# Performance work log

Measured on AMD Instinct MI355X. Metric: run time of the kernel, lower is better.

Reference implementation:

```python
import jax, jax.numpy as jnp
import numpy as np

HEADS = 24
HEAD_DIM = 128
DIM = HEADS * HEAD_DIM  # 3072
EPS = 1e-5


def _rms_norm(x, w):
    # x: [B,S,H,D], w: [D]
    var = jnp.mean(jnp.square(x), axis=-1, keepdims=True)
    return x * jax.lax.rsqrt(var + EPS) * w


def _apply_rope(x, cos, sin):
    # non-neox (interleaved pairs): x: [B,S,H,D], cos/sin: [S,D]
    B, S, H, D = x.shape
    xr = x.reshape(B, S, H, D // 2, 2)
    x_real, x_imag = xr[..., 0], xr[..., 1]
    rotated = jnp.stack([-x_imag, x_real], axis=-1).reshape(B, S, H, D)
    c = cos[None, :, None, :]
    s = sin[None, :, None, :]
    return x * c + rotated * s


def setup_inputs() -> dict:
    key = jax.random.key(0)
    ks = jax.random.split(key, 20)
    B, S_img, S_txt = 1, 2048, 512
    S = S_img + S_txt
    sc = 1.0 / np.sqrt(DIM)
    inp = {
        "x": jax.random.normal(ks[0], (B, S_img, DIM), jnp.float32),
        "encoder_hidden_states": jax.random.normal(ks[1], (B, S_txt, DIM), jnp.float32),
        "rope_cos": jax.random.uniform(ks[2], (S, HEAD_DIM), jnp.float32),
        "rope_sin": jax.random.uniform(ks[3], (S, HEAD_DIM), jnp.float32),
        # image-stream projections (bias=False)
        "wq": jax.random.normal(ks[4], (DIM, DIM), jnp.float32) * sc,
        "wk": jax.random.normal(ks[5], (DIM, DIM), jnp.float32) * sc,
        "wv": jax.random.normal(ks[6], (DIM, DIM), jnp.float32) * sc,
        # text-stream projections (added_proj_bias=True)
        "w_add_q": jax.random.normal(ks[7], (DIM, DIM), jnp.float32) * sc,
        "w_add_k": jax.random.normal(ks[8], (DIM, DIM), jnp.float32) * sc,
        "w_add_v": jax.random.normal(ks[9], (DIM, DIM), jnp.float32) * sc,
        "b_add_q": jax.random.normal(ks[10], (DIM,), jnp.float32) * 0.01,
        "b_add_k": jax.random.normal(ks[11], (DIM,), jnp.float32) * 0.01,
        "b_add_v": jax.random.normal(ks[12], (DIM,), jnp.float32) * 0.01,
        # per-head RMSNorm weights
        "norm_q_w": jnp.ones((HEAD_DIM,), jnp.float32),
        "norm_k_w": jnp.ones((HEAD_DIM,), jnp.float32),
        "norm_aq_w": jnp.ones((HEAD_DIM,), jnp.float32),
        "norm_ak_w": jnp.ones((HEAD_DIM,), jnp.float32),
        # output projections (out_bias=True)
        "w_out": jax.random.normal(ks[13], (DIM, DIM), jnp.float32) * sc,
        "b_out": jax.random.normal(ks[14], (DIM,), jnp.float32) * 0.01,
        "w_add_out": jax.random.normal(ks[15], (DIM, DIM), jnp.float32) * sc,
        "b_add_out": jax.random.normal(ks[16], (DIM,), jnp.float32) * 0.01,
    }
    return inp


def reference(x, encoder_hidden_states, rope_cos, rope_sin,
              wq, wk, wv, w_add_q, w_add_k, w_add_v,
              b_add_q, b_add_k, b_add_v,
              norm_q_w, norm_k_w, norm_aq_w, norm_ak_w,
              w_out, b_out, w_add_out, b_add_out):
    B, S_img, _ = x.shape
    S_txt = encoder_hidden_states.shape[1]

    def proj(h, w, b=None):
        y = jnp.einsum('bsd,ed->bse', h, w)
        return y if b is None else y + b

    def heads(t):
        return t.reshape(B, t.shape[1], HEADS, HEAD_DIM)

    q = _rms_norm(heads(proj(x, wq)), norm_q_w)
    k = _rms_norm(heads(proj(x, wk)), norm_k_w)
    v = heads(proj(x, wv))

    eq = _rms_norm(heads(proj(encoder_hidden_states, w_add_q, b_add_q)), norm_aq_w)
    ek = _rms_norm(heads(proj(encoder_hidden_states, w_add_k, b_add_k)), norm_ak_w)
    ev = heads(proj(encoder_hidden_states, w_add_v, b_add_v))

    # encoder tokens first, then image tokens
    q = jnp.concatenate([eq, q], axis=1)
    k = jnp.concatenate([ek, k], axis=1)
    v = jnp.concatenate([ev, v], axis=1)

    q = _apply_rope(q, rope_cos, rope_sin)
    k = _apply_rope(k, rope_cos, rope_sin)

    scale = 1.0 / np.sqrt(HEAD_DIM)
    scores = jnp.einsum('bqhd,bkhd->bhqk', q, k) * scale
    attn = jax.nn.softmax(scores, axis=-1)
    o = jnp.einsum('bhqk,bkhd->bqhd', attn, v)
    o = o.reshape(B, S_txt + S_img, DIM)

    enc_o, img_o = o[:, :S_txt], o[:, S_txt:]
    img_out = jnp.einsum('bsd,ed->bse', img_o, w_out) + b_out
    enc_out = jnp.einsum('bsd,ed->bse', enc_o, w_add_out) + b_add_out
    return img_out, enc_out
```

## Files before the change

### kernel.cpp

```cpp
#include <hip/hip_runtime.h>
#include <hip/hip_bf16.h>


typedef __hip_bfloat16 bf16;
typedef __attribute__((ext_vector_type(8))) short short8;
typedef __attribute__((ext_vector_type(4))) short s16x4;
typedef __attribute__((ext_vector_type(4))) float f32x4;

#define KDIM 3072
#define S_TXT 512
#define S_IMG 2048
#define S_ALL 2560
#define NHEADS 24
#define HDIM 128
#define WELEM (KDIM * KDIM)
#define AELEM (S_ALL * KDIM)
#define NSPLIT 3

__device__ __forceinline__ void async_ld16(const void* g, void* l) {
  __builtin_amdgcn_global_load_lds((__attribute__((address_space(1))) void*)g,
                                   (__attribute__((address_space(3))) void*)l,
                                   16, 0, 0);
}

__device__ __forceinline__ short bf16_bits(float x) {
  bf16 h = (bf16)x;
  return __builtin_bit_cast(short, h);
}
__device__ __forceinline__ float bits_f32(short s) {
  return (float)__builtin_bit_cast(bf16, s);
}

__global__ __launch_bounds__(256) void cast_weights_kernel(
    const float* __restrict__ w0, const float* __restrict__ w1,
    const float* __restrict__ w2, const float* __restrict__ w3,
    const float* __restrict__ w4, const float* __restrict__ w5,
    const float* __restrict__ w6, const float* __restrict__ w7,
    bf16* __restrict__ dst) {
  const float* srcs[8] = {w0, w1, w2, w3, w4, w5, w6, w7};
  const float* __restrict__ src = srcs[blockIdx.y];
  bf16* __restrict__ out = dst + (size_t)blockIdx.y * WELEM;
  const size_t i0 = ((size_t)blockIdx.x * 256 + threadIdx.x) * 8;
  const float4 f0 = *(const float4*)(src + i0);
  const float4 f1 = *(const float4*)(src + i0 + 4);
  short8 o;
  o[0] = bf16_bits(f0.x); o[1] = bf16_bits(f0.y);
  o[2] = bf16_bits(f0.z); o[3] = bf16_bits(f0.w);
  o[4] = bf16_bits(f1.x); o[5] = bf16_bits(f1.y);
  o[6] = bf16_bits(f1.z); o[7] = bf16_bits(f1.w);
  *(short8*)(out + i0) = o;
}

__global__ __launch_bounds__(256) void cast_acts_kernel(
    const float* __restrict__ x, const float* __restrict__ enc,
    bf16* __restrict__ xe) {
  const size_t i0 = ((size_t)blockIdx.x * 256 + threadIdx.x) * 8;
  const size_t TXT = (size_t)S_TXT * KDIM;
  const float* __restrict__ src = (i0 < TXT) ? (enc + i0) : (x + (i0 - TXT));
  const float4 f0 = *(const float4*)(src);
  const float4 f1 = *(const float4*)(src + 4);
  short8 o;
  o[0] = bf16_bits(f0.x); o[1] = bf16_bits(f0.y);
  o[2] = bf16_bits(f0.z); o[3] = bf16_bits(f0.w);
  o[4] = bf16_bits(f1.x); o[5] = bf16_bits(f1.y);
  o[6] = bf16_bits(f1.z); o[7] = bf16_bits(f1.w);
  *(short8*)(xe + i0) = o;
}

template <typename OutT, bool TRANS>
__device__ __forceinline__ void gemm_tile(const bf16* __restrict__ A,
                                          const bf16* __restrict__ B,
                                          OutT* __restrict__ C,
                                          const float* __restrict__ bias) {
  __shared__ alignas(16) short sA[128 * 32];
  __shared__ alignas(16) short sB[128 * 32];
  const int tid = threadIdx.x;
  const int lane = tid & 63;
  const int w = tid >> 6;
  const int a = lane & 15;
  const int g = lane >> 4;
  const int wm = (w >> 1) * 64;
  const int wn = (w & 1) * 64;

  f32x4 acc[4][4] = {};

  const int s0 = tid, s1 = tid + 256;
  const int r0 = s0 >> 2, b0 = (s0 & 3) ^ ((r0 >> 1) & 3);
  const int r1 = s1 >> 2, b1 = (s1 & 3) ^ ((r1 >> 1) & 3);
  const bf16* gA0 = A + (size_t)r0 * KDIM + b0 * 8;
  const bf16* gA1 = A + (size_t)r1 * KDIM + b1 * 8;
  const bf16* gB0 = B + (size_t)r0 * KDIM + b0 * 8;
  const bf16* gB1 = B + (size_t)r1 * KDIM + b1 * 8;
  short* lA0 = sA + (w * 64) * 8;
  short* lA1 = sA + (256 + w * 64) * 8;
  short* lB0 = sB + (w * 64) * 8;
  short* lB1 = sB + (256 + w * 64) * 8;

  for (int k0 = 0; k0 < KDIM; k0 += 32) {
    __syncthreads();
    async_ld16(gA0 + k0, lA0);
    async_ld16(gA1 + k0, lA1);
    async_ld16(gB0 + k0, lB0);
    async_ld16(gB1 + k0, lB1);
    __syncthreads();
    short8 af[4], bfg[4];
#pragma unroll
    for (int i = 0; i < 4; i++) {
      const int R = wm + i * 16 + a;
      af[i] = *(const short8*)(sA + R * 32 + ((g ^ ((R >> 1) & 3)) * 8));
    }
#pragma unroll
    for (int j = 0; j < 4; j++) {
      const int R = wn + j * 16 + a;
      bfg[j] = *(const short8*)(sB + R * 32 + ((g ^ ((R >> 1) & 3)) * 8));
    }
#pragma unroll
    for (int i = 0; i < 4; i++)
#pragma unroll
      for (int j = 0; j < 4; j++)
        acc[i][j] = __builtin_amdgcn_mfma_f32_16x16x32_bf16(af[i], bfg[j], acc[i][j], 0, 0, 0);
  }

  if constexpr (TRANS) {
#pragma unroll
    for (int i = 0; i < 4; i++)
#pragma unroll
      for (int j = 0; j < 4; j++) {
        const int col = wn + j * 16 + a;
        const float bv = bias ? bias[col] : 0.0f;
        s16x4 pk;
#pragma unroll
        for (int r = 0; r < 4; r++) pk[r] = bf16_bits(acc[i][j][r] + bv);
        *(s16x4*)((short*)C + (size_t)col * S_ALL + wm + i * 16 + g * 4) = pk;
      }
  } else {
#pragma unroll
    for (int i = 0; i < 4; i++)
#pragma unroll
      for (int j = 0; j < 4; j++) {
        const int col = wn + j * 16 + a;
        const float bv = bias ? bias[col] : 0.0f;
#pragma unroll
        for (int r = 0; r < 4; r++) {
          const int row = wm + i * 16 + g * 4 + r;
          C[(size_t)row * KDIM + col] = (OutT)(acc[i][j][r] + bv);
        }
      }
  }
}

__global__ __launch_bounds__(256) void qkv_kernel(
    const bf16* __restrict__ XE, const bf16* __restrict__ Wc,
    const float* __restrict__ bq, const float* __restrict__ bk, const float* __restrict__ bv,
    bf16* __restrict__ Q, bf16* __restrict__ K, bf16* __restrict__ VT) {
  const int bm = blockIdx.x;
  const int bn = blockIdx.y;
  const int which = bn / 24;
  const int nc = (bn % 24) * 128;
  const bool txt = bm < 4;
  const bf16* W = Wc + (size_t)(txt ? (3 + which) : which) * WELEM + (size_t)nc * KDIM;
  const float* bias = nullptr;
  if (txt) bias = ((which == 0) ? bq : (which == 1) ? bk : bv) + nc;
  const int crow = bm * 128;
  const bf16* A = XE + (size_t)crow * KDIM;
  if (which == 2) {
    gemm_tile<bf16, true>(A, W, VT + (size_t)nc * S_ALL + crow, bias);
  } else {
    bf16* Out = (which == 0) ? Q : K;
    gemm_tile<bf16, false>(A, W, Out + (size_t)crow * KDIM + nc, bias);
  }
}

__global__ __launch_bounds__(256) void outproj_kernel(
    const bf16* __restrict__ Obuf, const bf16* __restrict__ Wc,
    const float* __restrict__ b_out, const float* __restrict__ b_add,
    float* __restrict__ out) {
  const int bm = blockIdx.x;
  const int bn = blockIdx.y;
  const bool txt = bm < 4;
  const bf16* A = Obuf + (size_t)bm * 128 * KDIM;
  const bf16* W = Wc + (size_t)(txt ? 7 : 6) * WELEM;
  const float* bias = txt ? b_add : b_out;
  float* C = txt ? (out + (size_t)S_IMG * KDIM + (size_t)bm * 128 * KDIM)
                 : (out + (size_t)(bm - 4) * 128 * KDIM);
  gemm_tile<float, false>(A, W + (size_t)bn * 128 * KDIM, C + bn * 128, bias + bn * 128);
}

__global__ __launch_bounds__(256) void norm_rope_kernel(
    bf16* __restrict__ Q, bf16* __restrict__ K,
    const float* __restrict__ rc, const float* __restrict__ rs,
    const float* __restrict__ nqw, const float* __restrict__ nkw,
    const float* __restrict__ naqw, const float* __restrict__ nakw) {
  const int row = blockIdx.x;
  const int h = blockIdx.y * 4 + (threadIdx.x >> 6);
  const int t = threadIdx.x & 63;
  const long base = (long)row * KDIM + h * HDIM;
  const int d0 = 2 * t, d1 = d0 + 1;
  const bool txt = row < S_TXT;
  const float QSCL = 0.08838834764831845f * 1.4426950408889634f;
  float qa = (float)Q[base + d0], qb = (float)Q[base + d1];
  float ka = (float)K[base + d0], kb = (float)K[base + d1];
  float sq = qa * qa + qb * qb;
  float sk = ka * ka + kb * kb;
#pragma unroll
  for (int m = 1; m < 64; m <<= 1) {
    sq += __shfl_xor(sq, m);
    sk += __shfl_xor(sk, m);
  }
  const float rq = rsqrtf(sq * (1.0f / 128.0f) + 1e-5f) * QSCL;
  const float rk = rsqrtf(sk * (1.0f / 128.0f) + 1e-5f);
  const float* qw = txt ? naqw : nqw;
  const float* kw = txt ? nakw : nkw;
  const float c0 = rc[row * HDIM + d0], c1 = rc[row * HDIM + d1];
  const float s0 = rs[row * HDIM + d0], s1 = rs[row * HDIM + d1];
  const float qn0 = qa * rq * qw[d0], qn1 = qb * rq * qw[d1];
  const float kn0 = ka * rk * kw[d0], kn1 = kb * rk * kw[d1];
  Q[base + d0] = (bf16)(qn0 * c0 - qn1 * s0);
  Q[base + d1] = (bf16)(qn1 * c1 + qn0 * s1);
  K[base + d0] = (bf16)(kn0 * c0 - kn1 * s0);
  K[base + d1] = (bf16)(kn1 * c1 + kn0 * s1);
}

__global__ __launch_bounds__(256) void flash_kernel(
    const bf16* __restrict__ Q, const bf16* __restrict__ Kb,
    const bf16* __restrict__ VT,
    bf16* __restrict__ Op0, bf16* __restrict__ Op1, bf16* __restrict__ Op2,
    float* __restrict__ L) {
  __shared__ alignas(16) short sK[64 * 128];
  __shared__ alignas(16) short sVT[128 * 64];
  __shared__ alignas(16) short sP[4][32 * 72];
  const int tid = threadIdx.x;
  const int lane = tid & 63;
  const int w = tid >> 6;
  const int a = lane & 15;
  const int g = lane >> 4;
  const int qt = blockIdx.x;
  const int h = blockIdx.y;
  const int split = blockIdx.z;
  const int it0 = split * 13;
  const int it1 = (split == 2) ? 40 : (it0 + 13);
  const int qrow0 = qt * 128 + w * 32;
  short* const sPw = sP[w];

  short8 qf[2][4];
#pragma unroll
  for (int mi = 0; mi < 2; mi++)
#pragma unroll
    for (int kk = 0; kk < 4; kk++)
      qf[mi][kk] = *(const short8*)(Q + (size_t)(qrow0 + mi * 16 + a) * KDIM + h * HDIM + kk * 32 + g * 8);

  f32x4 oacc[2][8] = {};
  float lsum[2] = {0.0f, 0.0f};

  for (int it = it0; it < it1; ++it) {
    const int kv0 = it * 64;
    __syncthreads();
#pragma unroll
    for (int is = 0; is < 4; is++) {
      const int s = is * 256 + w * 64 + lane;
      const int kr = s >> 4, p = s & 15;
      const int lb = (p - (kr & 7)) & 15;
      async_ld16(Kb + (size_t)(kv0 + kr) * KDIM + h * HDIM + lb * 8,
                 sK + (is * 256 + w * 64) * 8);
    }
#pragma unroll
    for (int is = 0; is < 4; is++) {
      const int s = is * 256 + w * 64 + lane;
      const int dr = s >> 3, p = s & 7;
      const int lb = (p - (dr & 7)) & 7;
      async_ld16(VT + (size_t)(h * HDIM + dr) * S_ALL + kv0 + lb * 8,
                 sVT + (is * 256 + w * 64) * 8);
    }
    __syncthreads();

    f32x4 st[4][2] = {};
#pragma unroll
    for (int kk = 0; kk < 4; kk++) {
      short8 kf[4];
#pragma unroll
      for (int ni = 0; ni < 4; ni++) {
        const int kr = ni * 16 + a;
        const int p = ((kk * 4 + g) + (kr & 7)) & 15;
        kf[ni] = *(const short8*)(sK + kr * 128 + p * 8);
      }
#pragma unroll
      for (int ni = 0; ni < 4; ni++)
#pragma unroll
        for (int mi = 0; mi < 2; mi++)
          st[ni][mi] = __builtin_amdgcn_mfma_f32_16x16x32_bf16(kf[ni], qf[mi][kk], st[ni][mi], 0, 0, 0);
    }

#pragma unroll
    for (int mi = 0; mi < 2; mi++)
#pragma unroll
      for (int ni = 0; ni < 4; ni++) {
        s16x4 pk;
#pragma unroll
        for (int r = 0; r < 4; r++) {
          const float p = exp2f(st[ni][mi][r]);
          lsum[mi] += p;
          pk[r] = bf16_bits(p);
        }
        *(s16x4*)(sPw + (mi * 16 + a) * 72 + ni * 16 + g * 4) = pk;
      }

#pragma unroll
    for (int ks = 0; ks < 2; ks++) {
      short8 pf[2];
#pragma unroll
      for (int mi = 0; mi < 2; mi++)
        pf[mi] = *(const short8*)(sPw + (mi * 16 + a) * 72 + ks * 32 + g * 8);
#pragma unroll
      for (int nd = 0; nd < 8; nd++) {
        const int dr = nd * 16 + a;
        const int p = ((ks * 4 + g) + (dr & 7)) & 7;
        const short8 vf = *(const short8*)(sVT + dr * 64 + p * 8);
#pragma unroll
        for (int mi = 0; mi < 2; mi++)
          oacc[mi][nd] = __builtin_amdgcn_mfma_f32_16x16x32_bf16(pf[mi], vf, oacc[mi][nd], 0, 0, 0);
      }
    }
  }

#pragma unroll
  for (int mi = 0; mi < 2; mi++) {
    lsum[mi] += __shfl_xor(lsum[mi], 16);
    lsum[mi] += __shfl_xor(lsum[mi], 32);
  }
  bf16* __restrict__ Op = (split == 0) ? Op0 : (split == 1) ? Op1 : Op2;
#pragma unroll
  for (int mi = 0; mi < 2; mi++) {
#pragma unroll
    for (int r = 0; r < 4; r++) {
      const float inv = 1.0f / __shfl(lsum[mi], g * 4 + r);
      const size_t row = qrow0 + mi * 16 + g * 4 + r;
#pragma unroll
      for (int nd = 0; nd < 8; nd++)
        Op[row * KDIM + h * HDIM + nd * 16 + a] = (bf16)(oacc[mi][nd][r] * inv);
    }
    if (g == 0)
      L[((size_t)split * NHEADS + h) * S_ALL + qrow0 + mi * 16 + a] = lsum[mi];
  }
}

__global__ __launch_bounds__(256) void merge_kernel(
    bf16* __restrict__ O0, const bf16* __restrict__ O1, const bf16* __restrict__ O2,
    const float* __restrict__ L) {
  const size_t i0 = ((size_t)blockIdx.x * 256 + threadIdx.x) * 8;
  const int row = (int)(i0 / KDIM);
  const int h = (int)((i0 % KDIM) >> 7);
  const float l0 = L[((size_t)0 * NHEADS + h) * S_ALL + row];
  const float l1 = L[((size_t)1 * NHEADS + h) * S_ALL + row];
  const float l2 = L[((size_t)2 * NHEADS + h) * S_ALL + row];
  const float inv = 1.0f / (l0 + l1 + l2);
  const float w0 = l0 * inv, w1 = l1 * inv, w2 = l2 * inv;
  const short8 v0 = *(const short8*)(O0 + i0);
  const short8 v1 = *(const short8*)(O1 + i0);
  const short8 v2 = *(const short8*)(O2 + i0);
  short8 o;
#pragma unroll
  for (int u = 0; u < 8; u++)
    o[u] = bf16_bits(w0 * bits_f32(v0[u]) + w1 * bits_f32(v1[u]) + w2 * bits_f32(v2[u]));
  *(short8*)(O0 + i0) = o;
}

extern "C" void kernel_launch(void* const* d_in, const int* in_sizes, int n_in,
                              void* d_out, int out_size, void* d_ws, size_t ws_size,
                              hipStream_t stream) {
  const float* x    = (const float*)d_in[0];
  const float* enc  = (const float*)d_in[1];
  const float* rc   = (const float*)d_in[2];
  const float* rs   = (const float*)d_in[3];
  const float* wq   = (const float*)d_in[4];
  const float* wk   = (const float*)d_in[5];
  const float* wv   = (const float*)d_in[6];
  const float* waq  = (const float*)d_in[7];
  const float* wak  = (const float*)d_in[8];
  const float* wav  = (const float*)d_in[9];
  const float* bq   = (const float*)d_in[10];
  const float* bk   = (const float*)d_in[11];
  const float* bv   = (const float*)d_in[12];
  const float* nqw  = (const float*)d_in[13];
  const float* nkw  = (const float*)d_in[14];
  const float* naqw = (const float*)d_in[15];
  const float* nakw = (const float*)d_in[16];
  const float* w_out     = (const float*)d_in[17];
  const float* b_out     = (const float*)d_in[18];
  const float* w_add_out = (const float*)d_in[19];
  const float* b_add_out = (const float*)d_in[20];

  bf16* Wc   = (bf16*)d_ws;
  bf16* XE   = Wc + (size_t)8 * WELEM;
  bf16* Q    = XE + AELEM;
  bf16* K    = Q + AELEM;
  bf16* VT   = K + AELEM;
  bf16* Obuf = VT + AELEM;
  bf16* Op1  = Obuf + AELEM;
  bf16* Op2  = XE;
  float* L   = (float*)(Op1 + AELEM);

  cast_weights_kernel<<<dim3(WELEM / 2048, 8), 256, 0, stream>>>(
      wq, wk, wv, waq, wak, wav, w_out, w_add_out, Wc);
  cast_acts_kernel<<<dim3(AELEM / 2048), 256, 0, stream>>>(x, enc, XE);

  qkv_kernel<<<dim3(20, 72), 256, 0, stream>>>(XE, Wc, bq, bk, bv, Q, K, VT);
  norm_rope_kernel<<<dim3(S_ALL, 6), 256, 0, stream>>>(Q, K, rc, rs, nqw, nkw, naqw, nakw);
  flash_kernel<<<dim3(20, NHEADS, NSPLIT), 256, 0, stream>>>(Q, K, VT, Obuf, Op1, Op2, L);
  merge_kernel<<<dim3(AELEM / 2048), 256, 0, stream>>>(Obuf, Op1, Op2, L);
  outproj_kernel<<<dim3(20, NHEADS), 256, 0, stream>>>(Obuf, Wc, b_out, b_add_out,
                                                       (float*)d_out);
}
```

Before: 754.0 us.

## Rewrite QKV GEMM as 256x256 tiled, 8-wave pipelined kernel with XCD block remap

```diff
diff --git a/kernel.cpp b/kernel.cpp
--- a/kernel.cpp
+++ b/kernel.cpp
@@ -16,6 +16,7 @@
 #define WELEM (KDIM * KDIM)
 #define AELEM (S_ALL * KDIM)
 #define NSPLIT 3
+#define NT_K 48
 
 __device__ __forceinline__ void async_ld16(const void* g, void* l) {
   __builtin_amdgcn_global_load_lds((__attribute__((address_space(1))) void*)g,
@@ -29,6 +30,17 @@
 }
 __device__ __forceinline__ float bits_f32(short s) {
   return (float)__builtin_bit_cast(bf16, s);
+}
+
+__device__ __forceinline__ void phase_mid() {
+  __builtin_amdgcn_s_barrier();
+  asm volatile("s_waitcnt lgkmcnt(0)" ::: "memory");
+  __builtin_amdgcn_sched_barrier(0);
+  __builtin_amdgcn_s_setprio(1);
+}
+__device__ __forceinline__ void phase_end() {
+  __builtin_amdgcn_s_setprio(0);
+  __builtin_amdgcn_s_barrier();
 }
 
 __global__ __launch_bounds__(256) void cast_weights_kernel(
@@ -68,6 +80,175 @@
 }
 
 template <typename OutT, bool TRANS>
+__device__ __forceinline__ void gemm256(const bf16* __restrict__ Ab,
+                                        const bf16* __restrict__ Bb,
+                                        OutT* __restrict__ C,
+                                        const float* __restrict__ bias,
+                                        short* sAmem, short* sBmem) {
+  const int tid = threadIdx.x;
+  const int lane = tid & 63;
+  const int w = tid >> 6;
+  const int a = lane & 15;
+  const int g = (lane >> 4) & 3;
+  const int wm = w >> 2;
+  const int wn = w & 3;
+
+  short* const A00 = sAmem;
+  short* const A01 = sAmem + 8192;
+  short* const A10 = sAmem + 16384;
+  short* const A11 = sAmem + 24576;
+  short* const B00 = sBmem;
+  short* const B01 = sBmem + 8192;
+  short* const B10 = sBmem + 16384;
+  short* const B11 = sBmem + 24576;
+
+  auto stage = [&](const bf16* gb, int kbase, short* lblk) {
+#pragma unroll
+    for (int l = 0; l < 2; l++) {
+      const int t = l * 512 + tid;
+      const int row = t >> 2;
+      const int ls = (t & 3) ^ ((row >> 1) & 3);
+      async_ld16(gb + (size_t)row * KDIM + kbase + ls * 8,
+                 lblk + (l * 512 + w * 64) * 8);
+    }
+  };
+  auto frag = [&](const short* lblk, int R) -> short8 {
+    return *(const short8*)(lblk + R * 32 + ((g ^ ((R >> 1) & 3)) * 8));
+  };
+
+  f32x4 acc[8][4] = {};
+
+  stage(Bb, 0, B00);
+  stage(Ab, 0, A00);
+  stage(Bb, 32, B01);
+  stage(Ab, 32, A01);
+  stage(Bb, 64, B10);
+  stage(Ab, 64, A10);
+  stage(Bb, 96, B11);
+  asm volatile("s_waitcnt vmcnt(6)" ::: "memory");
+  __builtin_amdgcn_s_barrier();
+
+  const int ra = wm * 128 + a;
+  const int rb = wn * 64 + a;
+
+  auto kblock = [&](int u, short* cA0, short* cA1, short* cB0, short* cB1,
+                    short* nA1) {
+    short8 af[4], bfr[4];
+#pragma unroll
+    for (int i = 0; i < 4; i++) af[i] = frag(cA0, ra + i * 16);
+#pragma unroll
+    for (int j = 0; j < 4; j++) bfr[j] = frag(cB0, rb + j * 16);
+    if (u + 1 < NT_K) stage(Ab, (u + 1) * 64 + 32, nA1);
+    phase_mid();
+#pragma unroll
+    for (int i = 0; i < 4; i++)
+#pragma unroll
+      for (int j = 0; j < 4; j++)
+        acc[i][j] = __builtin_amdgcn_mfma_f32_16x16x32_bf16(af[i], bfr[j], acc[i][j], 0, 0, 0);
+    phase_end();
+#pragma unroll
+    for (int i = 0; i < 4; i++) af[i] = frag(cA0, ra + (i + 4) * 16);
+    if (u + 2 < NT_K) stage(Bb, (u + 2) * 64, cB0);
+    phase_mid();
+#pragma unroll
+    for (int i = 0; i < 4; i++)
+#pragma unroll
+      for (int j = 0; j < 4; j++)
+        acc[i + 4][j] = __builtin_amdgcn_mfma_f32_16x16x32_bf16(af[i], bfr[j], acc[i + 4][j], 0, 0, 0);
+    phase_end();
+#pragma unroll
+    for (int i = 0; i < 4; i++) af[i] = frag(cA1, ra + i * 16);
+#pragma unroll
+    for (int j = 0; j < 4; j++) bfr[j] = frag(cB1, rb + j * 16);
+    if (u + 2 < NT_K) stage(Ab, (u + 2) * 64, cA0);
+    phase_mid();
+#pragma unroll
+    for (int i = 0; i < 4; i++)
+#pragma unroll
+      for (int j = 0; j < 4; j++)
+        acc[i][j] = __builtin_amdgcn_mfma_f32_16x16x32_bf16(af[i], bfr[j], acc[i][j], 0, 0, 0);
+    phase_end();
+#pragma unroll
+    for (int i = 0; i < 4; i++) af[i] = frag(cA1, ra + (i + 4) * 16);
+    if (u + 2 < NT_K) stage(Bb, (u + 2) * 64 + 32, cB1);
+    __builtin_amdgcn_s_barrier();
+    asm volatile("s_waitcnt lgkmcnt(0)" ::: "memory");
+    __builtin_amdgcn_sched_barrier(0);
+    __builtin_amdgcn_s_setprio(1);
+#pragma unroll
+    for (int i = 0; i < 4; i++)
+#pragma unroll
+      for (int j = 0; j < 4; j++)
+        acc[i + 4][j] = __builtin_amdgcn_mfma_f32_16x16x32_bf16(af[i], bfr[j], acc[i + 4][j], 0, 0, 0);
+    __builtin_amdgcn_s_setprio(0);
+    if (u < NT_K - 2)
+      asm volatile("s_waitcnt vmcnt(6)" ::: "memory");
+    else
+      asm volatile("s_waitcnt vmcnt(0)" ::: "memory");
+    __builtin_amdgcn_s_barrier();
+  };
+
+#pragma unroll 1
+  for (int u = 0; u < NT_K; u += 2) {
+    kblock(u,     A00, A01, B00, B01, A11);
+    kblock(u + 1, A10, A11, B10, B11, A01);
+  }
+
+  if constexpr (TRANS) {
+#pragma unroll
+    for (int i = 0; i < 8; i++)
+#pragma unroll
+      for (int j = 0; j < 4; j++) {
+        const int col = wn * 64 + j * 16 + a;
+        const float bv = bias ? bias[col] : 0.0f;
+        s16x4 pk;
+#pragma unroll
+        for (int r = 0; r < 4; r++) pk[r] = bf16_bits(acc[i][j][r] + bv);
+        *(s16x4*)((short*)C + (size_t)col * S_ALL + wm * 128 + i * 16 + g * 4) = pk;
+      }
+  } else {
+#pragma unroll
+    for (int i = 0; i < 8; i++)
+#pragma unroll
+      for (int j = 0; j < 4; j++) {
+        const int col = wn * 64 + j * 16 + a;
+        const float bv = bias ? bias[col] : 0.0f;
+#pragma unroll
+        for (int r = 0; r < 4; r++) {
+          const int row = wm * 128 + i * 16 + g * 4 + r;
+          C[(size_t)row * KDIM + col] = (OutT)(acc[i][j][r] + bv);
+        }
+      }
+  }
+}
+
+__global__ __launch_bounds__(512, 2) void qkv_kernel(
+    const bf16* __restrict__ XE, const bf16* __restrict__ Wc,
+    const float* __restrict__ bq, const float* __restrict__ bk, const float* __restrict__ bv,
+    bf16* __restrict__ Q, bf16* __restrict__ K, bf16* __restrict__ VT) {
+  __shared__ alignas(16) short sAmem[4 * 8192];
+  __shared__ alignas(16) short sBmem[4 * 8192];
+  const int bid = blockIdx.x;
+  const int wk_ = (bid & 7) * 45 + (bid >> 3);
+  const int bm = wk_ / 36;
+  const int bn = wk_ % 36;
+  const int which = bn / 12;
+  const int nc = (bn % 12) * 256;
+  const bool txt = bm < 2;
+  const bf16* W = Wc + (size_t)(txt ? (3 + which) : which) * WELEM + (size_t)nc * KDIM;
+  const float* bias = nullptr;
+  if (txt) bias = ((which == 0) ? bq : (which == 1) ? bk : bv) + nc;
+  const int crow = bm * 256;
+  const bf16* A = XE + (size_t)crow * KDIM;
+  if (which == 2) {
+    gemm256<bf16, true>(A, W, VT + (size_t)nc * S_ALL + crow, bias, sAmem, sBmem);
+  } else {
+    bf16* Out = (which == 0) ? Q : K;
+    gemm256<bf16, false>(A, W, Out + (size_t)crow * KDIM + nc, bias, sAmem, sBmem);
+  }
+}
+
+template <typename OutT, bool TRANS>
 __device__ __forceinline__ void gemm_tile(const bf16* __restrict__ A,
                                           const bf16* __restrict__ B,
                                           OutT* __restrict__ C,
@@ -146,28 +327,6 @@
           C[(size_t)row * KDIM + col] = (OutT)(acc[i][j][r] + bv);
         }
       }
-  }
-}
-
-__global__ __launch_bounds__(256) void qkv_kernel(
-    const bf16* __restrict__ XE, const bf16* __restrict__ Wc,
-    const float* __restrict__ bq, const float* __restrict__ bk, const float* __restrict__ bv,
-    bf16* __restrict__ Q, bf16* __restrict__ K, bf16* __restrict__ VT) {
-  const int bm = blockIdx.x;
-  const int bn = blockIdx.y;
-  const int which = bn / 24;
-  const int nc = (bn % 24) * 128;
-  const bool txt = bm < 4;
-  const bf16* W = Wc + (size_t)(txt ? (3 + which) : which) * WELEM + (size_t)nc * KDIM;
-  const float* bias = nullptr;
-  if (txt) bias = ((which == 0) ? bq : (which == 1) ? bk : bv) + nc;
-  const int crow = bm * 128;
-  const bf16* A = XE + (size_t)crow * KDIM;
-  if (which == 2) {
-    gemm_tile<bf16, true>(A, W, VT + (size_t)nc * S_ALL + crow, bias);
-  } else {
-    bf16* Out = (which == 0) ? Q : K;
-    gemm_tile<bf16, false>(A, W, Out + (size_t)crow * KDIM + nc, bias);
   }
 }
 
@@ -403,7 +562,7 @@
       wq, wk, wv, waq, wak, wav, w_out, w_add_out, Wc);
   cast_acts_kernel<<<dim3(AELEM / 2048), 256, 0, stream>>>(x, enc, XE);
 
-  qkv_kernel<<<dim3(20, 72), 256, 0, stream>>>(XE, Wc, bq, bk, bv, Q, K, VT);
+  qkv_kernel<<<dim3(360), dim3(512), 0, stream>>>(XE, Wc, bq, bk, bv, Q, K, VT);
   norm_rope_kernel<<<dim3(S_ALL, 6), 256, 0, stream>>>(Q, K, rc, rs, nqw, nkw, naqw, nakw);
   flash_kernel<<<dim3(20, NHEADS, NSPLIT), 256, 0, stream>>>(Q, K, VT, Obuf, Op1, Op2, L);
   merge_kernel<<<dim3(AELEM / 2048), 256, 0, stream>>>(Obuf, Op1, Op2, L);
```

After: 754.3 us. No clear change (+0.0%).
